# Kernel tuning notes

Measured on AMD Instinct MI355X. Metric: run time of the kernel, lower is better.

The kernel has to match this reference:

```python
import jax, jax.numpy as jnp
import numpy as np

NUM_HEADS = 16
CAUSAL = True


def setup_inputs() -> dict:
    key = jax.random.key(0)
    ks = jax.random.split(key, 3)
    B, T, D = 2, 2048, 1024
    s = 1.0 / np.sqrt(D)
    return {
        "x": jax.random.normal(ks[0], (B, T, D), dtype=jnp.float32),
        "W_qkv": jax.random.normal(ks[1], (3 * D, D), dtype=jnp.float32) * s,
        "b_qkv": jnp.zeros((3 * D,), dtype=jnp.float32),
        "W_out": jax.random.normal(ks[2], (D, D), dtype=jnp.float32) * s,
        "b_out": jnp.zeros((D,), dtype=jnp.float32),
    }


def reference(x, W_qkv, b_qkv, W_out, b_out):
    B, T, D = x.shape
    H = NUM_HEADS
    hd = D // H
    # qkv projection: torch Linear y = x @ W.T + b
    qkv = jnp.einsum('btd,ed->bte', x, W_qkv) + b_qkv  # [B,T,3D]
    qkv = qkv.reshape(B, T, H, 3 * hd).transpose(0, 2, 1, 3)  # [B,H,T,3hd]
    q, k, v = jnp.split(qkv, 3, axis=-1)  # each [B,H,T,hd]
    scale = 1.0 / np.sqrt(hd).astype(np.float32)
    scores = jnp.einsum('bhtd,bhsd->bhts', q, k) * scale  # [B,H,T,T]
    if CAUSAL:
        mask = jnp.triu(jnp.ones((T, T), dtype=bool), k=1)
        scores = jnp.where(mask, jnp.float32(-jnp.inf), scores)
    weights = jax.nn.softmax(scores, axis=-1)
    attn = jnp.einsum('bhts,bhsd->bhtd', weights, v)  # [B,H,T,hd]
    out = attn.transpose(0, 2, 1, 3).reshape(B, T, D)
    return jnp.einsum('btd,ed->bte', out, W_out) + b_out
```

## Files before the change

kernel.cpp:

```cpp
#include <hip/hip_runtime.h>
#include <hip/hip_bf16.h>
#include <cstdint>


using short8  = __attribute__((ext_vector_type(8))) short;
using floatx4 = __attribute__((ext_vector_type(4))) float;

#define LDS_STRIDE 40

__device__ __forceinline__ float bf16_to_f32(unsigned short u) {
    union { unsigned int i; float f; } v; v.i = ((unsigned int)u) << 16; return v.f;
}
__device__ __forceinline__ unsigned short f32_to_bf16(float f) {
    union { float f; unsigned int i; } v; v.f = f;
    unsigned int x = v.i;
    unsigned int r = x + 0x7FFFu + ((x >> 16) & 1u);
    return (unsigned short)(r >> 16);
}
__device__ __forceinline__ unsigned short f32_to_bf16_fast(float f) {
    union { float f; unsigned int i; } v; v.f = f;
    return (unsigned short)((v.i + 0x8000u) >> 16);
}
__device__ __forceinline__ short8 cvt8(const float* __restrict__ p) {
    const float4 f0 = *(const float4*)p;
    const float4 f1 = *(const float4*)(p + 4);
    short8 r;
    r[0] = (short)f32_to_bf16(f0.x); r[1] = (short)f32_to_bf16(f0.y);
    r[2] = (short)f32_to_bf16(f0.z); r[3] = (short)f32_to_bf16(f0.w);
    r[4] = (short)f32_to_bf16(f1.x); r[5] = (short)f32_to_bf16(f1.y);
    r[6] = (short)f32_to_bf16(f1.z); r[7] = (short)f32_to_bf16(f1.w);
    return r;
}
__device__ __forceinline__ unsigned int cvtpk(float a, float b) {
    unsigned int r;
    asm("v_cvt_pk_bf16_f32 %0, %1, %2" : "=v"(r) : "v"(a), "v"(b));
    return r;
}

#define Q_PRESCALE 0.1803368801111204f

#if __has_builtin(__builtin_amdgcn_global_load_lds)
#define ASYNC_STAGE 1
typedef const __attribute__((address_space(1))) void* gas1_t;
typedef __attribute__((address_space(3))) void* las3_t;
#else
#define ASYNC_STAGE 0
#endif

__device__ __forceinline__ void gload_lds16(const ushort* g, ushort* l) {
#if ASYNC_STAGE
    __builtin_amdgcn_global_load_lds((gas1_t)g, (las3_t)l, 16, 0, 0);
#else
    *(short8*)l = *(const short8*)g;
#endif
}

__global__ __launch_bounds__(256, 8) void cvt_bf16_3(
    const float* __restrict__ x,  const float* __restrict__ wq,
    const float* __restrict__ wo, ushort* __restrict__ xb,
    ushort* __restrict__ wqb, ushort* __restrict__ wob)
{
    const int i = blockIdx.x * 256 + threadIdx.x;
    const float* src; ushort* dst; int off;
    if (i < 524288)      { src = x;  dst = xb;  off = i; }
    else if (i < 917504) { src = wq; dst = wqb; off = i - 524288; }
    else                 { src = wo; dst = wob; off = i - 917504; }
    *(short8*)(dst + (size_t)off * 8) = cvt8(src + (size_t)off * 8);
}

template <int MODE>
__global__ __launch_bounds__(256, 3) void gemm_bf16(
    const ushort* __restrict__ A, const ushort* __restrict__ W,
    const float* __restrict__ bias,
    ushort* __restrict__ Cq, ushort* __restrict__ Ck, ushort* __restrict__ Cv,
    float* __restrict__ Cout, int M, int N, int K)
{
    __shared__ __align__(16) ushort As[128 * 32];
    __shared__ __align__(16) ushort Bs[128 * 32];

    const int tid  = threadIdx.x;
    const int lane = tid & 63;
    const int wave = tid >> 6;
    const int wm = (wave >> 1) * 64;
    const int wn = (wave & 1) * 64;
    const int m0 = blockIdx.x * 128;
    const int n0 = blockIdx.y * 128;
    const int quad = lane >> 4;
    const int l16  = lane & 15;

    floatx4 acc[4][4];
#pragma unroll
    for (int i = 0; i < 4; i++)
#pragma unroll
        for (int j = 0; j < 4; j++) acc[i][j] = (floatx4)0.0f;

    const int srow = wave * 16 + (lane >> 2);
    const int scol = (lane & 3) * 8;
    ushort* ldsA0 = &As[wave * 512];
    ushort* ldsA1 = &As[2048 + wave * 512];
    ushort* ldsB0 = &Bs[wave * 512];
    ushort* ldsB1 = &Bs[2048 + wave * 512];
    const ushort* pA0 = A + (size_t)(m0 + srow) * K + scol;
    const ushort* pA1 = pA0 + (size_t)64 * K;
    const ushort* pB0 = W + (size_t)(n0 + srow) * K + scol;
    const ushort* pB1 = pB0 + (size_t)64 * K;

    for (int k0 = 0; k0 < K; k0 += 32) {
#if ASYNC_STAGE
        __syncthreads();
        gload_lds16(pA0 + k0, ldsA0);
        gload_lds16(pA1 + k0, ldsA1);
        gload_lds16(pB0 + k0, ldsB0);
        gload_lds16(pB1 + k0, ldsB1);
        __syncthreads();
#else
        const short8 a0 = *(const short8*)(pA0 + k0);
        const short8 a1 = *(const short8*)(pA1 + k0);
        const short8 b0 = *(const short8*)(pB0 + k0);
        const short8 b1 = *(const short8*)(pB1 + k0);
        __syncthreads();
        *(short8*)&As[srow * 32 + scol] = a0;
        *(short8*)&As[(srow + 64) * 32 + scol] = a1;
        *(short8*)&Bs[srow * 32 + scol] = b0;
        *(short8*)&Bs[(srow + 64) * 32 + scol] = b1;
        __syncthreads();
#endif

        short8 af[4], bf[4];
#pragma unroll
        for (int i = 0; i < 4; i++)
            af[i] = *(const short8*)&As[(wm + i * 16 + l16) * 32 + quad * 8];
#pragma unroll
        for (int j = 0; j < 4; j++)
            bf[j] = *(const short8*)&Bs[(wn + j * 16 + l16) * 32 + quad * 8];
#pragma unroll
        for (int i = 0; i < 4; i++)
#pragma unroll
            for (int j = 0; j < 4; j++)
                acc[i][j] = __builtin_amdgcn_mfma_f32_16x16x32_bf16(af[i], bf[j], acc[i][j], 0, 0, 0);
    }

#pragma unroll
    for (int i = 0; i < 4; i++) {
#pragma unroll
        for (int j = 0; j < 4; j++) {
#pragma unroll
            for (int r = 0; r < 4; r++) {
                const int row = m0 + wm + i * 16 + quad * 4 + r;
                const int col = n0 + wn + j * 16 + l16;
                float v = acc[i][j][r] + bias[col];
                if (MODE == 0) {
                    const int h  = col / 192;
                    const int rr = col - h * 192;
                    const int sel = rr >> 6;
                    const int d   = rr & 63;
                    const int b = row >> 11;
                    const int t = row & 2047;
                    const size_t idx = (((size_t)(b * 16 + h)) * 2048 + t) * 64 + d;
                    if (sel == 0)      Cq[idx] = f32_to_bf16(v * Q_PRESCALE);
                    else if (sel == 1) Ck[idx] = f32_to_bf16(v);
                    else               Cv[idx] = f32_to_bf16(v);
                } else {
                    Cout[(size_t)row * N + col] = v;
                }
            }
        }
    }
}

template <int MODE, int AFP32>
__global__ __launch_bounds__(256, 2) void gemm_bt(
    const void* __restrict__ Av, const float* __restrict__ W,
    const float* __restrict__ bias,
    ushort* __restrict__ Cq, ushort* __restrict__ Ck, ushort* __restrict__ Cv,
    float* __restrict__ Cout, int M, int N, int K)
{
    __shared__ __align__(16) ushort As[128 * LDS_STRIDE];
    __shared__ __align__(16) ushort Bs[128 * LDS_STRIDE];

    const int tid  = threadIdx.x;
    const int lane = tid & 63;
    const int wave = tid >> 6;
    const int wm = (wave >> 1) * 64;
    const int wn = (wave & 1) * 64;
    const int m0 = blockIdx.x * 128;
    const int n0 = blockIdx.y * 128;
    const int quad = lane >> 4;
    const int l16  = lane & 15;

    floatx4 acc[4][4];
#pragma unroll
    for (int i = 0; i < 4; i++)
#pragma unroll
        for (int j = 0; j < 4; j++) acc[i][j] = (floatx4)0.0f;

    const int srow = tid >> 2;
    const int scol = (tid & 3) * 8;

    for (int k0 = 0; k0 < K; k0 += 32) {
        short8 a0, a1;
        if (AFP32) {
            const float* A = (const float*)Av;
            a0 = cvt8(A + (size_t)(m0 + srow) * K + k0 + scol);
            a1 = cvt8(A + (size_t)(m0 + srow + 64) * K + k0 + scol);
        } else {
            const ushort* A = (const ushort*)Av;
            a0 = *(const short8*)(A + (size_t)(m0 + srow) * K + k0 + scol);
            a1 = *(const short8*)(A + (size_t)(m0 + srow + 64) * K + k0 + scol);
        }
        const short8 b0 = cvt8(W + (size_t)(n0 + srow) * K + k0 + scol);
        const short8 b1 = cvt8(W + (size_t)(n0 + srow + 64) * K + k0 + scol);
        __syncthreads();
        *(short8*)&As[srow * LDS_STRIDE + scol] = a0;
        *(short8*)&As[(srow + 64) * LDS_STRIDE + scol] = a1;
        *(short8*)&Bs[srow * LDS_STRIDE + scol] = b0;
        *(short8*)&Bs[(srow + 64) * LDS_STRIDE + scol] = b1;
        __syncthreads();

        short8 af[4], bf[4];
#pragma unroll
        for (int i = 0; i < 4; i++)
            af[i] = *(const short8*)&As[(wm + i * 16 + l16) * LDS_STRIDE + quad * 8];
#pragma unroll
        for (int j = 0; j < 4; j++)
            bf[j] = *(const short8*)&Bs[(wn + j * 16 + l16) * LDS_STRIDE + quad * 8];
#pragma unroll
        for (int i = 0; i < 4; i++)
#pragma unroll
            for (int j = 0; j < 4; j++)
                acc[i][j] = __builtin_amdgcn_mfma_f32_16x16x32_bf16(af[i], bf[j], acc[i][j], 0, 0, 0);
    }

#pragma unroll
    for (int i = 0; i < 4; i++) {
#pragma unroll
        for (int j = 0; j < 4; j++) {
#pragma unroll
            for (int r = 0; r < 4; r++) {
                const int row = m0 + wm + i * 16 + quad * 4 + r;
                const int col = n0 + wn + j * 16 + l16;
                float v = acc[i][j][r] + bias[col];
                if (MODE == 0) {
                    const int h  = col / 192;
                    const int rr = col - h * 192;
                    const int sel = rr >> 6;
                    const int d   = rr & 63;
                    const int b = row >> 11;
                    const int t = row & 2047;
                    const size_t idx = (((size_t)(b * 16 + h)) * 2048 + t) * 64 + d;
                    if (sel == 0)      Cq[idx] = f32_to_bf16(v * Q_PRESCALE);
                    else if (sel == 1) Ck[idx] = f32_to_bf16(v);
                    else               Cv[idx] = f32_to_bf16(v);
                } else {
                    Cout[(size_t)row * N + col] = v;
                }
            }
        }
    }
}

__global__ __launch_bounds__(256, 4) void transpose_v(
    const ushort* __restrict__ V, ushort* __restrict__ Vt)
{
    const int bh = blockIdx.x & 31;
    const int tt = blockIdx.x >> 5;
    const int t0 = tt * 64;
    const int tid = threadIdx.x;
    __shared__ __align__(16) ushort tile[64 * 72];

    const int r = tid >> 2, c = (tid & 3) * 16;
    const ushort* src = V + ((size_t)bh * 2048 + t0 + r) * 64 + c;
    *(short8*)&tile[r * 72 + c]     = *(const short8*)src;
    *(short8*)&tile[r * 72 + c + 8] = *(const short8*)(src + 8);
    __syncthreads();

    const int w = tid >> 6, lane = tid & 63;
    const int d  = w * 16 + (lane >> 2);
    const int tc = (lane & 3) * 16;
    __attribute__((aligned(16))) ushort out[16];
#pragma unroll
    for (int i = 0; i < 16; i++) {
        const int slot = (tc & 31) + i;
        const int key  = ((slot >> 2) & 1) * 16 + ((slot >> 3) & 3) * 4 + (slot & 3);
        out[i] = tile[((tc & 32) + key) * 72 + d];
    }
    ushort* dst = Vt + ((size_t)(bh * 32 + tt) * 64 + d) * 64 + tc;
    *(short8*)dst       = *(const short8*)&out[0];
    *(short8*)(dst + 8) = *(const short8*)&out[8];
}

__global__ __launch_bounds__(256, 2) void attn_mfma(
    const ushort* __restrict__ Q, const ushort* __restrict__ K,
    const ushort* __restrict__ Vtb, ushort* __restrict__ O)
{
    const int bid   = blockIdx.x;
    const int bh    = bid & 31;
    const int qtIdx = bid >> 5;
    const int qt    = (qtIdx < 8) ? (15 - qtIdx) : (qtIdx - 8);
    const int tid  = threadIdx.x;
    const int wave = tid >> 6;
    const int lane = tid & 63;
    const int quad = lane >> 4;
    const int l16  = lane & 15;
    const int qb   = qt * 128 + wave * 32;

    __shared__ __align__(16) ushort Ks[2][4096];
    __shared__ __align__(16) ushort Vs[2][4096];

    const size_t kbase = (size_t)bh * 2048 * 64;

    const int ob0 = tid * 16, ob1 = ob0 + 4096;
    const int r0 = ob0 >> 7, c0 = (ob0 >> 4) & 7;
    const int r1 = ob1 >> 7, c1 = (ob1 >> 4) & 7;
    const int e0 = r0 * 64 + ((c0 ^ (r0 & 7)) << 3);
    const int e1 = r1 * 64 + ((c1 ^ (r1 & 7)) << 3);
    const ushort* Kb = K + kbase;
    const ushort* Vb = Vtb + (size_t)bh * 32 * 4096;

    auto stage = [&](int t, ushort* KsB, ushort* VsB) {
        const ushort* Ktile = Kb + t * 4096;
        const ushort* Vtile = Vb + t * 4096;
        gload_lds16(Ktile + e0, KsB + wave * 512);
        gload_lds16(Ktile + e1, KsB + 2048 + wave * 512);
        gload_lds16(Vtile + e0, VsB + wave * 512);
        gload_lds16(Vtile + e1, VsB + 2048 + wave * 512);
    };

    const int sw0 = ((quad ^ (l16 & 7)) << 3);
    const int sw1 = (((4 + quad) ^ (l16 & 7)) << 3);
    const int rbase = l16 * 64;

    short8 qf0[2], qf1[2];
#pragma unroll
    for (int f = 0; f < 2; f++) {
        const ushort* qp = Q + kbase + (size_t)(qb + f * 16 + l16) * 64 + quad * 8;
        qf0[f] = *(const short8*)qp;
        qf1[f] = *(const short8*)(qp + 32);
    }

    floatx4 accO[2][4];
#pragma unroll
    for (int f = 0; f < 2; f++)
#pragma unroll
        for (int d = 0; d < 4; d++) accO[f][d] = (floatx4)0.0f;
    float accLs[2] = {0.0f, 0.0f};

    union PB { unsigned int u[4]; short8 s8; };

    auto compute = [&](int t, const ushort* KsB, const ushort* VsB) {
        short8 kf[4][2], vf[4][2];
#pragma unroll
        for (int j = 0; j < 4; j++) {
            kf[j][0] = *(const short8*)&KsB[j * 1024 + rbase + sw0];
            kf[j][1] = *(const short8*)&KsB[j * 1024 + rbase + sw1];
        }
#pragma unroll
        for (int d = 0; d < 4; d++) {
            vf[d][0] = *(const short8*)&VsB[d * 1024 + rbase + sw0];
            vf[d][1] = *(const short8*)&VsB[d * 1024 + rbase + sw1];
        }

#pragma unroll
        for (int f = 0; f < 2; f++) {
            const int qlo = qb + f * 16;
            if (t * 64 > qlo + 15) continue;
            floatx4 s[4];
#pragma unroll
            for (int j = 0; j < 4; j++) {
                floatx4 acc = (floatx4)0.0f;
                acc = __builtin_amdgcn_mfma_f32_16x16x32_bf16(kf[j][0], qf0[f], acc, 0, 0, 0);
                acc = __builtin_amdgcn_mfma_f32_16x16x32_bf16(kf[j][1], qf1[f], acc, 0, 0, 0);
                s[j] = acc;
            }
            if (t * 64 + 63 > qlo) {
                const int qcol = qlo + l16;
#pragma unroll
                for (int j = 0; j < 4; j++) {
                    const int keyb = t * 64 + j * 16 + quad * 4;
#pragma unroll
                    for (int r = 0; r < 4; r++)
                        if (keyb + r > qcol) s[j][r] = -1e30f;
                }
            }
#pragma unroll
            for (int j = 0; j < 4; j++)
#pragma unroll
                for (int r = 0; r < 4; r++)
                    s[j][r] = __builtin_amdgcn_exp2f(s[j][r]);
            const floatx4 ssum = s[0] + s[1] + s[2] + s[3];
            accLs[f] += (ssum[0] + ssum[1]) + (ssum[2] + ssum[3]);
            PB p0, p1;
#pragma unroll
            for (int j = 0; j < 2; j++) {
                p0.u[j * 2 + 0] = cvtpk(s[j][0], s[j][1]);
                p0.u[j * 2 + 1] = cvtpk(s[j][2], s[j][3]);
                p1.u[j * 2 + 0] = cvtpk(s[j + 2][0], s[j + 2][1]);
                p1.u[j * 2 + 1] = cvtpk(s[j + 2][2], s[j + 2][3]);
            }
#pragma unroll
            for (int d = 0; d < 4; d++) {
                accO[f][d] = __builtin_amdgcn_mfma_f32_16x16x32_bf16(p0.s8, vf[d][0], accO[f][d], 0, 0, 0);
                accO[f][d] = __builtin_amdgcn_mfma_f32_16x16x32_bf16(p1.s8, vf[d][1], accO[f][d], 0, 0, 0);
            }
        }
    };

    const int nt = 2 * qt + 2;
    stage(0, Ks[0], Vs[0]);
    __syncthreads();
    int t = 0;
    while (true) {
        if (t + 1 < nt) stage(t + 1, Ks[1], Vs[1]);
        compute(t, Ks[0], Vs[0]);
        __syncthreads();
        if (++t >= nt) break;
        if (t + 1 < nt) stage(t + 1, Ks[0], Vs[0]);
        compute(t, Ks[1], Vs[1]);
        __syncthreads();
        if (++t >= nt) break;
    }

    const int b = bh >> 4, h = bh & 15;
#pragma unroll
    for (int f = 0; f < 2; f++) {
        float L = accLs[f];
        L += __shfl_xor(L, 16);
        L += __shfl_xor(L, 32);
        float inv[4];
#pragma unroll
        for (int r = 0; r < 4; r++) inv[r] = 1.0f / __shfl(L, quad * 4 + r);
#pragma unroll
        for (int d = 0; d < 4; d++)
#pragma unroll
            for (int r = 0; r < 4; r++)
                O[(size_t)(b * 2048 + qb + f * 16 + quad * 4 + r) * 1024 + h * 64 + d * 16 + l16] =
                    f32_to_bf16(accO[f][d][r] * inv[r]);
    }
}

extern "C" void kernel_launch(void* const* d_in, const int* in_sizes, int n_in,
                              void* d_out, int out_size, void* d_ws, size_t ws_size,
                              hipStream_t stream) {
    const float* x    = (const float*)d_in[0];
    const float* Wqkv = (const float*)d_in[1];
    const float* bqkv = (const float*)d_in[2];
    const float* Wout = (const float*)d_in[3];
    const float* bout = (const float*)d_in[4];
    float* out = (float*)d_out;

    char* ws = (char*)d_ws;
    const size_t MB = 1024 * 1024;
    ushort* Q    = (ushort*)(ws + 0 * MB);
    ushort* Kk   = (ushort*)(ws + 8 * MB);
    ushort* Vt   = (ushort*)(ws + 16 * MB);
    ushort* rawV = (ushort*)(ws + 24 * MB);
    ushort* O    = (ushort*)(ws + 24 * MB);

    const dim3 blk(256);
    if (ws_size >= 48 * MB) {
        ushort* xb    = (ushort*)(ws + 32 * MB);
        ushort* Wqkvb = (ushort*)(ws + 40 * MB);
        ushort* Woutb = (ushort*)(ws + 46 * MB);
        cvt_bf16_3<<<dim3(4096), blk, 0, stream>>>(x, Wqkv, Wout, xb, Wqkvb, Woutb);
        gemm_bf16<0><<<dim3(32, 24), blk, 0, stream>>>(xb, Wqkvb, bqkv, Q, Kk, rawV,
                                                       nullptr, 4096, 3072, 1024);
        transpose_v<<<dim3(1024), blk, 0, stream>>>(rawV, Vt);
        attn_mfma<<<dim3(512), blk, 0, stream>>>(Q, Kk, Vt, O);
        gemm_bf16<1><<<dim3(32, 8), blk, 0, stream>>>(O, Woutb, bout, nullptr, nullptr,
                                                      nullptr, out, 4096, 1024, 1024);
    } else {
        gemm_bt<0, 1><<<dim3(32, 24), blk, 0, stream>>>(x, Wqkv, bqkv, Q, Kk, rawV,
                                                        nullptr, 4096, 3072, 1024);
        transpose_v<<<dim3(1024), blk, 0, stream>>>(rawV, Vt);
        attn_mfma<<<dim3(512), blk, 0, stream>>>(Q, Kk, Vt, O);
        gemm_bt<1, 0><<<dim3(32, 8), blk, 0, stream>>>(O, Wout, bout, nullptr, nullptr,
                                                       nullptr, out, 4096, 1024, 1024);
    }
}
```

Before: 177.5 us.

## Fuse V transpose into QKV GEMM epilogue and stage 128-key tiles in attention

The QKV projection epilogue now writes V straight into the transposed, key-permuted tile layout that attention consumes, so the separate transpose_v kernel and its extra global round trip go away. The attention kernel also stages two 64-key sub-tiles per pipeline step, which halves the number of barriers and doubles the LDS footprint. The scattered V stores in the GEMM epilogue may coalesce worse, and the larger LDS use may reduce occupancy.

```diff
diff --git a/kernel.cpp b/kernel.cpp
--- a/kernel.cpp
+++ b/kernel.cpp
@@ -16,10 +16,6 @@
     unsigned int x = v.i;
     unsigned int r = x + 0x7FFFu + ((x >> 16) & 1u);
     return (unsigned short)(r >> 16);
-}
-__device__ __forceinline__ unsigned short f32_to_bf16_fast(float f) {
-    union { float f; unsigned int i; } v; v.f = f;
-    return (unsigned short)((v.i + 0x8000u) >> 16);
 }
 __device__ __forceinline__ short8 cvt8(const float* __restrict__ p) {
     const float4 f0 = *(const float4*)p;
@@ -53,6 +49,11 @@
 #else
     *(short8*)l = *(const short8*)g;
 #endif
+}
+
+__device__ __forceinline__ int v_slot(int k) {
+    const int k5 = k & 31;
+    return (k & 32) + ((k5 >> 4) & 1) * 4 + ((k5 >> 2) & 3) * 8 + (k5 & 3);
 }
 
 __global__ __launch_bounds__(256, 8) void cvt_bf16_3(
@@ -156,10 +157,16 @@
                     const int d   = rr & 63;
                     const int b = row >> 11;
                     const int t = row & 2047;
-                    const size_t idx = (((size_t)(b * 16 + h)) * 2048 + t) * 64 + d;
-                    if (sel == 0)      Cq[idx] = f32_to_bf16(v * Q_PRESCALE);
-                    else if (sel == 1) Ck[idx] = f32_to_bf16(v);
-                    else               Cv[idx] = f32_to_bf16(v);
+                    const int bh = b * 16 + h;
+                    if (sel == 0) {
+                        Cq[(((size_t)bh) * 2048 + t) * 64 + d] =
+                            f32_to_bf16(v * Q_PRESCALE);
+                    } else if (sel == 1) {
+                        Ck[(((size_t)bh) * 2048 + t) * 64 + d] = f32_to_bf16(v);
+                    } else {
+                        Cv[(((size_t)bh * 32 + (t >> 6)) * 64 + d) * 64 + v_slot(t & 63)] =
+                            f32_to_bf16(v);
+                    }
                 } else {
                     Cout[(size_t)row * N + col] = v;
                 }
@@ -247,46 +254,22 @@
                     const int d   = rr & 63;
                     const int b = row >> 11;
                     const int t = row & 2047;
-                    const size_t idx = (((size_t)(b * 16 + h)) * 2048 + t) * 64 + d;
-                    if (sel == 0)      Cq[idx] = f32_to_bf16(v * Q_PRESCALE);
-                    else if (sel == 1) Ck[idx] = f32_to_bf16(v);
-                    else               Cv[idx] = f32_to_bf16(v);
+                    const int bh = b * 16 + h;
+                    if (sel == 0) {
+                        Cq[(((size_t)bh) * 2048 + t) * 64 + d] =
+                            f32_to_bf16(v * Q_PRESCALE);
+                    } else if (sel == 1) {
+                        Ck[(((size_t)bh) * 2048 + t) * 64 + d] = f32_to_bf16(v);
+                    } else {
+                        Cv[(((size_t)bh * 32 + (t >> 6)) * 64 + d) * 64 + v_slot(t & 63)] =
+                            f32_to_bf16(v);
+                    }
                 } else {
                     Cout[(size_t)row * N + col] = v;
                 }
             }
         }
     }
-}
-
-__global__ __launch_bounds__(256, 4) void transpose_v(
-    const ushort* __restrict__ V, ushort* __restrict__ Vt)
-{
-    const int bh = blockIdx.x & 31;
-    const int tt = blockIdx.x >> 5;
-    const int t0 = tt * 64;
-    const int tid = threadIdx.x;
-    __shared__ __align__(16) ushort tile[64 * 72];
-
-    const int r = tid >> 2, c = (tid & 3) * 16;
-    const ushort* src = V + ((size_t)bh * 2048 + t0 + r) * 64 + c;
-    *(short8*)&tile[r * 72 + c]     = *(const short8*)src;
-    *(short8*)&tile[r * 72 + c + 8] = *(const short8*)(src + 8);
-    __syncthreads();
-
-    const int w = tid >> 6, lane = tid & 63;
-    const int d  = w * 16 + (lane >> 2);
-    const int tc = (lane & 3) * 16;
-    __attribute__((aligned(16))) ushort out[16];
-#pragma unroll
-    for (int i = 0; i < 16; i++) {
-        const int slot = (tc & 31) + i;
-        const int key  = ((slot >> 2) & 1) * 16 + ((slot >> 3) & 3) * 4 + (slot & 3);
-        out[i] = tile[((tc & 32) + key) * 72 + d];
-    }
-    ushort* dst = Vt + ((size_t)(bh * 32 + tt) * 64 + d) * 64 + tc;
-    *(short8*)dst       = *(const short8*)&out[0];
-    *(short8*)(dst + 8) = *(const short8*)&out[8];
 }
 
 __global__ __launch_bounds__(256, 2) void attn_mfma(
@@ -304,26 +287,33 @@
     const int l16  = lane & 15;
     const int qb   = qt * 128 + wave * 32;
 
-    __shared__ __align__(16) ushort Ks[2][4096];
-    __shared__ __align__(16) ushort Vs[2][4096];
+    __shared__ __align__(16) ushort Ks[2][8192];
+    __shared__ __align__(16) ushort Vs[2][8192];
 
     const size_t kbase = (size_t)bh * 2048 * 64;
 
-    const int ob0 = tid * 16, ob1 = ob0 + 4096;
-    const int r0 = ob0 >> 7, c0 = (ob0 >> 4) & 7;
-    const int r1 = ob1 >> 7, c1 = (ob1 >> 4) & 7;
-    const int e0 = r0 * 64 + ((c0 ^ (r0 & 7)) << 3);
-    const int e1 = r1 * 64 + ((c1 ^ (r1 & 7)) << 3);
+    int e[4];
+#pragma unroll
+    for (int c = 0; c < 4; c++) {
+        const int ob  = tid * 16 + c * 4096;
+        const int sub = ob >> 13;
+        const int obs = ob & 8191;
+        const int r   = obs >> 7;
+        const int ch  = (obs >> 4) & 7;
+        e[c] = sub * 4096 + r * 64 + ((ch ^ (r & 7)) << 3);
+    }
     const ushort* Kb = K + kbase;
     const ushort* Vb = Vtb + (size_t)bh * 32 * 4096;
 
-    auto stage = [&](int t, ushort* KsB, ushort* VsB) {
-        const ushort* Ktile = Kb + t * 4096;
-        const ushort* Vtile = Vb + t * 4096;
-        gload_lds16(Ktile + e0, KsB + wave * 512);
-        gload_lds16(Ktile + e1, KsB + 2048 + wave * 512);
-        gload_lds16(Vtile + e0, VsB + wave * 512);
-        gload_lds16(Vtile + e1, VsB + 2048 + wave * 512);
+    auto stage = [&](int t128, ushort* KsB, ushort* VsB) {
+        const ushort* Ktile = Kb + t128 * 8192;
+        const ushort* Vtile = Vb + t128 * 8192;
+#pragma unroll
+        for (int c = 0; c < 4; c++)
+            gload_lds16(Ktile + e[c], KsB + c * 2048 + wave * 512);
+#pragma unroll
+        for (int c = 0; c < 4; c++)
+            gload_lds16(Vtile + e[c], VsB + c * 2048 + wave * 512);
     };
 
     const int sw0 = ((quad ^ (l16 & 7)) << 3);
@@ -347,65 +337,72 @@
 
     union PB { unsigned int u[4]; short8 s8; };
 
-    auto compute = [&](int t, const ushort* KsB, const ushort* VsB) {
-        short8 kf[4][2], vf[4][2];
-#pragma unroll
-        for (int j = 0; j < 4; j++) {
-            kf[j][0] = *(const short8*)&KsB[j * 1024 + rbase + sw0];
-            kf[j][1] = *(const short8*)&KsB[j * 1024 + rbase + sw1];
-        }
-#pragma unroll
-        for (int d = 0; d < 4; d++) {
-            vf[d][0] = *(const short8*)&VsB[d * 1024 + rbase + sw0];
-            vf[d][1] = *(const short8*)&VsB[d * 1024 + rbase + sw1];
-        }
-
-#pragma unroll
-        for (int f = 0; f < 2; f++) {
-            const int qlo = qb + f * 16;
-            if (t * 64 > qlo + 15) continue;
-            floatx4 s[4];
+    auto compute = [&](int t128, const ushort* KsB, const ushort* VsB) {
+#pragma unroll
+        for (int s = 0; s < 2; ++s) {
+            const int t64 = 2 * t128 + s;
+            if (t64 * 64 > qb + 31) continue;
+            const ushort* Kt = KsB + s * 4096;
+            const ushort* Vt = VsB + s * 4096;
+            short8 kf[4][2], vf[4][2];
 #pragma unroll
             for (int j = 0; j < 4; j++) {
-                floatx4 acc = (floatx4)0.0f;
-                acc = __builtin_amdgcn_mfma_f32_16x16x32_bf16(kf[j][0], qf0[f], acc, 0, 0, 0);
-                acc = __builtin_amdgcn_mfma_f32_16x16x32_bf16(kf[j][1], qf1[f], acc, 0, 0, 0);
-                s[j] = acc;
+                kf[j][0] = *(const short8*)&Kt[j * 1024 + rbase + sw0];
+                kf[j][1] = *(const short8*)&Kt[j * 1024 + rbase + sw1];
             }
-            if (t * 64 + 63 > qlo) {
-                const int qcol = qlo + l16;
+#pragma unroll
+            for (int d = 0; d < 4; d++) {
+                vf[d][0] = *(const short8*)&Vt[d * 1024 + rbase + sw0];
+                vf[d][1] = *(const short8*)&Vt[d * 1024 + rbase + sw1];
+            }
+
+#pragma unroll
+            for (int f = 0; f < 2; f++) {
+                const int qlo = qb + f * 16;
+                if (t64 * 64 > qlo + 15) continue;
+                floatx4 sc[4];
 #pragma unroll
                 for (int j = 0; j < 4; j++) {
-                    const int keyb = t * 64 + j * 16 + quad * 4;
+                    floatx4 acc = (floatx4)0.0f;
+                    acc = __builtin_amdgcn_mfma_f32_16x16x32_bf16(kf[j][0], qf0[f], acc, 0, 0, 0);
+                    acc = __builtin_amdgcn_mfma_f32_16x16x32_bf16(kf[j][1], qf1[f], acc, 0, 0, 0);
+                    sc[j] = acc;
+                }
+                if (t64 * 64 + 63 > qlo) {
+                    const int qcol = qlo + l16;
+#pragma unroll
+                    for (int j = 0; j < 4; j++) {
+                        const int keyb = t64 * 64 + j * 16 + quad * 4;
+#pragma unroll
+                        for (int r = 0; r < 4; r++)
+                            if (keyb + r > qcol) sc[j][r] = -1e30f;
+                    }
+                }
+#pragma unroll
+                for (int j = 0; j < 4; j++)
 #pragma unroll
                     for (int r = 0; r < 4; r++)
-                        if (keyb + r > qcol) s[j][r] = -1e30f;
-                }
-            }
-#pragma unroll
-            for (int j = 0; j < 4; j++)
-#pragma unroll
-                for (int r = 0; r < 4; r++)
-                    s[j][r] = __builtin_amdgcn_exp2f(s[j][r]);
-            const floatx4 ssum = s[0] + s[1] + s[2] + s[3];
-            accLs[f] += (ssum[0] + ssum[1]) + (ssum[2] + ssum[3]);
-            PB p0, p1;
-#pragma unroll
-            for (int j = 0; j < 2; j++) {
-                p0.u[j * 2 + 0] = cvtpk(s[j][0], s[j][1]);
-                p0.u[j * 2 + 1] = cvtpk(s[j][2], s[j][3]);
-                p1.u[j * 2 + 0] = cvtpk(s[j + 2][0], s[j + 2][1]);
-                p1.u[j * 2 + 1] = cvtpk(s[j + 2][2], s[j + 2][3]);
-            }
-#pragma unroll
-            for (int d = 0; d < 4; d++) {
-                accO[f][d] = __builtin_amdgcn_mfma_f32_16x16x32_bf16(p0.s8, vf[d][0], accO[f][d], 0, 0, 0);
-                accO[f][d] = __builtin_amdgcn_mfma_f32_16x16x32_bf16(p1.s8, vf[d][1], accO[f][d], 0, 0, 0);
+                        sc[j][r] = __builtin_amdgcn_exp2f(sc[j][r]);
+                const floatx4 ssum = sc[0] + sc[1] + sc[2] + sc[3];
+                accLs[f] += (ssum[0] + ssum[1]) + (ssum[2] + ssum[3]);
+                PB p0, p1;
+#pragma unroll
+                for (int j = 0; j < 2; j++) {
+                    p0.u[j * 2 + 0] = cvtpk(sc[j][0], sc[j][1]);
+                    p0.u[j * 2 + 1] = cvtpk(sc[j][2], sc[j][3]);
+                    p1.u[j * 2 + 0] = cvtpk(sc[j + 2][0], sc[j + 2][1]);
+                    p1.u[j * 2 + 1] = cvtpk(sc[j + 2][2], sc[j + 2][3]);
+                }
+#pragma unroll
+                for (int d = 0; d < 4; d++) {
+                    accO[f][d] = __builtin_amdgcn_mfma_f32_16x16x32_bf16(p0.s8, vf[d][0], accO[f][d], 0, 0, 0);
+                    accO[f][d] = __builtin_amdgcn_mfma_f32_16x16x32_bf16(p1.s8, vf[d][1], accO[f][d], 0, 0, 0);
+                }
             }
         }
     };
 
-    const int nt = 2 * qt + 2;
+    const int nt = qt + 1;
     stage(0, Ks[0], Vs[0]);
     __syncthreads();
     int t = 0;
@@ -452,8 +449,7 @@
     const size_t MB = 1024 * 1024;
     ushort* Q    = (ushort*)(ws + 0 * MB);
     ushort* Kk   = (ushort*)(ws + 8 * MB);
-    ushort* Vt   = (ushort*)(ws + 16 * MB);
-    ushort* rawV = (ushort*)(ws + 24 * MB);
+    ushort* Vtb  = (ushort*)(ws + 16 * MB);
     ushort* O    = (ushort*)(ws + 24 * MB);
 
     const dim3 blk(256);
@@ -462,17 +458,15 @@
         ushort* Wqkvb = (ushort*)(ws + 40 * MB);
         ushort* Woutb = (ushort*)(ws + 46 * MB);
         cvt_bf16_3<<<dim3(4096), blk, 0, stream>>>(x, Wqkv, Wout, xb, Wqkvb, Woutb);
-        gemm_bf16<0><<<dim3(32, 24), blk, 0, stream>>>(xb, Wqkvb, bqkv, Q, Kk, rawV,
+        gemm_bf16<0><<<dim3(32, 24), blk, 0, stream>>>(xb, Wqkvb, bqkv, Q, Kk, Vtb,
                                                        nullptr, 4096, 3072, 1024);
-        transpose_v<<<dim3(1024), blk, 0, stream>>>(rawV, Vt);
-        attn_mfma<<<dim3(512), blk, 0, stream>>>(Q, Kk, Vt, O);
+        attn_mfma<<<dim3(512), blk, 0, stream>>>(Q, Kk, Vtb, O);
         gemm_bf16<1><<<dim3(32, 8), blk, 0, stream>>>(O, Woutb, bout, nullptr, nullptr,
                                                       nullptr, out, 4096, 1024, 1024);
     } else {
-        gemm_bt<0, 1><<<dim3(32, 24), blk, 0, stream>>>(x, Wqkv, bqkv, Q, Kk, rawV,
+        gemm_bt<0, 1><<<dim3(32, 24), blk, 0, stream>>>(x, Wqkv, bqkv, Q, Kk, Vtb,
                                                         nullptr, 4096, 3072, 1024);
-        transpose_v<<<dim3(1024), blk, 0, stream>>>(rawV, Vt);
-        attn_mfma<<<dim3(512), blk, 0, stream>>>(Q, Kk, Vt, O);
+        attn_mfma<<<dim3(512), blk, 0, stream>>>(Q, Kk, Vtb, O);
         gemm_bt<1, 0><<<dim3(32, 8), blk, 0, stream>>>(O, Wout, bout, nullptr, nullptr,
                                                        nullptr, out, 4096, 1024, 1024);
     }
```

After: 173.1 us. 1.03x faster.
